# Performance work log

Measured on AMD Instinct MI355X. Metric: run time of the kernel, lower is better.

## Reference

```python
import jax, jax.numpy as jnp
import numpy as np

X_DIM, Z_DIM, N_HEIGHT = 256, 256, 32
EPS = 1e-5  # BatchNorm1d eps

def _bn(x, g, b):
    # BatchNorm1d in training mode: batch statistics over the point axis
    m = x.mean(0)
    v = x.var(0)
    return (x - m) * jax.lax.rsqrt(v + EPS) * g + b

def setup_inputs() -> dict:
    key = jax.random.key(0)
    ks = jax.random.split(key, 16)
    B, N, F = 2, 120000, 3
    inp = {
        'pt_fea': jax.random.normal(ks[0], (B, N, F), jnp.float32),
        'grid_ind': jax.random.randint(ks[1], (B, N, 2), 0, 256, dtype=jnp.int32).astype(jnp.int64),
        'occupancy': (jax.random.uniform(ks[2], (B, 1, X_DIM, N_HEIGHT, Z_DIM)) < 0.1).astype(jnp.float32),
    }
    dims = [(3, 64), (64, 128), (128, 256), (256, 512)]
    for i, (di, do) in enumerate(dims):
        inp[f'W{i+1}'] = jax.random.normal(ks[3 + i], (di, do), jnp.float32) * 0.02
        inp[f'b{i+1}'] = jnp.zeros((do,), jnp.float32)
    for i, d in enumerate([3, 64, 128, 256]):
        inp[f'g{i}'] = jnp.ones((d,), jnp.float32)
        inp[f'be{i}'] = jnp.zeros((d,), jnp.float32)
    inp['Wc'] = jax.random.normal(ks[10], (512, 32), jnp.float32) * 0.02
    inp['bc'] = jnp.zeros((32,), jnp.float32)
    return inp

def reference(pt_fea, occupancy, W1, b1, W2, b2, W3, b3, W4, b4,
              g0, be0, g1, be1, g2, be2, g3, be3, Wc, bc, grid_ind):
    B, N, F = pt_fea.shape
    feats = pt_fea.reshape(B * N, F)                          # cat over batch
    # PointNet per-point MLP: BN -> (Linear -> BN -> ReLU) x3 -> Linear
    h = _bn(feats, g0, be0)
    h = jax.nn.relu(_bn(h @ W1 + b1, g1, be1))
    h = jax.nn.relu(_bn(h @ W2 + b2, g2, be2))
    h = jax.nn.relu(_bn(h @ W3 + b3, g3, be3))
    h = h @ W4 + b4                                           # [B*N, 512]

    # linear segment id per (batch, x, z) cell; equivalent to unique+scatter_max
    gi = grid_ind.reshape(B * N, 2).astype(jnp.int32)
    batch_idx = jnp.repeat(jnp.arange(B, dtype=jnp.int32), N)
    seg = batch_idx * (X_DIM * Z_DIM) + gi[:, 0] * Z_DIM + gi[:, 1]
    n_cells = B * X_DIM * Z_DIM

    pooled = jax.ops.segment_max(h, seg, num_segments=n_cells)          # [cells, 512]
    cnt = jax.ops.segment_sum(jnp.ones((B * N,), h.dtype), seg, num_segments=n_cells)
    occ_mask = (cnt > 0)[:, None]
    pooled = jnp.where(occ_mask, pooled, 0.0)                           # kill -inf empties

    # feature compression on occupied cells only; empty cells stay exactly 0
    comp = jax.nn.relu(pooled @ Wc + bc)
    comp = jnp.where(occ_mask, comp, 0.0)                               # [cells, 32]

    bev = comp.reshape(B, X_DIM, Z_DIM, -1).transpose(0, 3, 1, 2)       # [B, 32, X, Z]
    # MaxPool2d(k=3, stride=1, pad=1); -inf padding matches torch's implicit -inf pad
    bev = jax.lax.reduce_window(bev, -jnp.inf, jax.lax.max,
                                (1, 1, 3, 3), (1, 1, 1, 1), 'SAME')

    occu = occupancy[:, 0].transpose(0, 2, 1, 3)                        # [B, H, X, Z]
    out = jnp.concatenate([occu, bev], axis=1)                          # [B, H+32, X, Z]
    return out
```

## Files before the change

### kernel.cpp

```cpp
#include <hip/hip_runtime.h>
#include <hip/hip_bf16.h>

#define EPSN 1e-5f

typedef __bf16 bf16x8 __attribute__((ext_vector_type(8)));
typedef float f32x4 __attribute__((ext_vector_type(4)));

__device__ __forceinline__ unsigned encf(float f) {
  unsigned u = __float_as_uint(f);
  return (u & 0x80000000u) ? ~u : (u | 0x80000000u);
}
__device__ __forceinline__ float decf(unsigned u) {
  return (u & 0x80000000u) ? __uint_as_float(u ^ 0x80000000u) : __uint_as_float(~u);
}

__global__ __launch_bounds__(256) void stats_feats(const float* __restrict__ pt, int n,
                                                   float* __restrict__ sums) {
  float a0 = 0, a1 = 0, a2 = 0, q0 = 0, q1 = 0, q2 = 0;
  for (int p = blockIdx.x * 256 + threadIdx.x; p < n; p += gridDim.x * 256) {
    float v0 = pt[3 * p], v1 = pt[3 * p + 1], v2 = pt[3 * p + 2];
    a0 += v0; a1 += v1; a2 += v2;
    q0 += v0 * v0; q1 += v1 * v1; q2 += v2 * v2;
  }
  __shared__ float red[4][6];
  float vals[6] = {a0, a1, a2, q0, q1, q2};
  int lane = threadIdx.x & 63, wv = threadIdx.x >> 6;
#pragma unroll
  for (int k = 0; k < 6; k++) {
    float v = vals[k];
#pragma unroll
    for (int o = 32; o; o >>= 1) v += __shfl_down(v, o, 64);
    if (lane == 0) red[wv][k] = v;
  }
  __syncthreads();
  if (threadIdx.x < 6) {
    float v = red[0][threadIdx.x] + red[1][threadIdx.x] + red[2][threadIdx.x] + red[3][threadIdx.x];
    atomicAdd(&sums[threadIdx.x], v);
  }
}

__global__ void bn_prep(const float* __restrict__ sums, int C, float invN,
                        const float* __restrict__ g, const float* __restrict__ be,
                        float* __restrict__ sc, float* __restrict__ sh) {
  int c = threadIdx.x;
  if (c < C) {
    float m = sums[c] * invN;
    float v = fmaxf(sums[C + c] * invN - m * m, 0.f);
    float s = g[c] * rsqrtf(v + EPSN);
    sc[c] = s;
    sh[c] = be[c] - m * s;
  }
}

__global__ __launch_bounds__(256) void wconv(const float* __restrict__ W,
                                             __hip_bfloat16* __restrict__ Wt, int K, int C) {
  int idx = blockIdx.x * 256 + threadIdx.x;
  if (idx >= K * C) return;
  int k = idx / C, c = idx - k * C;
  Wt[(size_t)c * K + k] = __float2bfloat16(W[idx]);
}

__global__ __launch_bounds__(256) void gemm1_stats(const float* __restrict__ pt,
                                                   const float* __restrict__ W,
                                                   const float* __restrict__ bias,
                                                   const float* __restrict__ scsh,
                                                   __hip_bfloat16* __restrict__ Y,
                                                   int n, float* __restrict__ sums) {
  const int c = threadIdx.x & 63;
  const float w0 = W[c], w1 = W[64 + c], w2 = W[128 + c], bb = bias[c];
  const float s0 = scsh[0], s1 = scsh[1], s2 = scsh[2];
  const float h0 = scsh[4], h1 = scsh[5], h2 = scsh[6];
  float s = 0.f, q = 0.f;
  const int total = n * 64;
  for (int idx = blockIdx.x * 256 + threadIdx.x; idx < total; idx += gridDim.x * 256) {
    int p = idx >> 6;
    float x0 = s0 * pt[3 * p]     + h0;
    float x1 = s1 * pt[3 * p + 1] + h1;
    float x2 = s2 * pt[3 * p + 2] + h2;
    float y = bb + x0 * w0 + x1 * w1 + x2 * w2;
    Y[idx] = __float2bfloat16(y);
    s += y; q += y * y;
  }
  __shared__ float sred[4][64], qred[4][64];
  int wv = threadIdx.x >> 6;
  sred[wv][c] = s; qred[wv][c] = q;
  __syncthreads();
  if (threadIdx.x < 64) {
    float S = sred[0][c] + sred[1][c] + sred[2][c] + sred[3][c];
    float Q = qred[0][c] + qred[1][c] + qred[2][c] + qred[3][c];
    atomicAdd(&sums[c], S);
    atomicAdd(&sums[64 + c], Q);
  }
}

template <int K>
__global__ __launch_bounds__(256) void gemm_mfma(
    const __hip_bfloat16* __restrict__ Yin, const __hip_bfloat16* __restrict__ Wt,
    const float* __restrict__ bias, const float* __restrict__ sc, const float* __restrict__ sh,
    __hip_bfloat16* __restrict__ Yout, int C, float* __restrict__ sums, int nrows,
    const unsigned* __restrict__ perm) {
  constexpr int KS = 64, LDA = 72, LDO = 80;
  __shared__ __align__(16) __hip_bfloat16 hA[128 * LDO];
  __shared__ float sredArr[128], qredArr[128];
  const int t = threadIdx.x;
  const int lane = t & 63, wv = t >> 6;
  const int mh = (wv >> 1) * 64, nh = (wv & 1) * 64;
  const int lm = lane & 15, lq = lane >> 4;
  const int p0 = blockIdx.x * 128;
  const int cb0 = blockIdx.y * 128;

  f32x4 acc[4][4];
#pragma unroll
  for (int i = 0; i < 4; i++)
#pragma unroll
    for (int j = 0; j < 4; j++) acc[i][j] = {0.f, 0.f, 0.f, 0.f};

  for (int k0 = 0; k0 < K; k0 += KS) {
    __syncthreads();
#pragma unroll
    for (int it = 0; it < 4; it++) {
      int idx = it * 256 + t;
      int row = idx >> 3;
      int c8 = (idx & 7) * 8;
      int gp = p0 + row;
      __hip_bfloat16 h8[8];
      if (gp < nrows) {
        uint4 raw = *(const uint4*)(Yin + (size_t)gp * K + k0 + c8);
        const __hip_bfloat16* pr = (const __hip_bfloat16*)&raw;
#pragma unroll
        for (int j = 0; j < 8; j++) {
          float v = sc[k0 + c8 + j] * __bfloat162float(pr[j]) + sh[k0 + c8 + j];
          h8[j] = __float2bfloat16(fmaxf(v, 0.f));
        }
      } else {
#pragma unroll
        for (int j = 0; j < 8; j++) h8[j] = __float2bfloat16(0.f);
      }
      *(uint4*)&hA[row * LDA + c8] = *(const uint4*)h8;
    }
    __syncthreads();
#pragma unroll
    for (int kk = 0; kk < KS; kk += 32) {
      bf16x8 a[4], b[4];
#pragma unroll
      for (int i = 0; i < 4; i++)
        a[i] = *(const bf16x8*)&hA[(mh + i * 16 + lm) * LDA + kk + lq * 8];
#pragma unroll
      for (int j = 0; j < 4; j++)
        b[j] = *(const bf16x8*)(const void*)(Wt + (size_t)(cb0 + nh + j * 16 + lm) * K + k0 + kk + lq * 8);
#pragma unroll
      for (int i = 0; i < 4; i++)
#pragma unroll
        for (int j = 0; j < 4; j++)
          acc[i][j] = __builtin_amdgcn_mfma_f32_16x16x32_bf16(a[i], b[j], acc[i][j], 0, 0, 0);
    }
  }

#pragma unroll
  for (int j = 0; j < 4; j++) {
    float bb = bias[cb0 + nh + j * 16 + lm];
#pragma unroll
    for (int i = 0; i < 4; i++)
#pragma unroll
      for (int r = 0; r < 4; r++) acc[i][j][r] += bb;
  }

  __syncthreads();
  if (t < 128) { sredArr[t] = 0.f; qredArr[t] = 0.f; }
  __syncthreads();

#pragma unroll
  for (int j = 0; j < 4; j++) {
    float s = 0.f, q = 0.f;
#pragma unroll
    for (int i = 0; i < 4; i++)
#pragma unroll
      for (int r = 0; r < 4; r++) {
        int grow = p0 + mh + i * 16 + lq * 4 + r;
        if (grow < nrows) { float v = acc[i][j][r]; s += v; q += v * v; }
      }
    s += __shfl_xor(s, 16); s += __shfl_xor(s, 32);
    q += __shfl_xor(q, 16); q += __shfl_xor(q, 32);
    if (lq == 0) {
      atomicAdd(&sredArr[nh + j * 16 + lm], s);
      atomicAdd(&qredArr[nh + j * 16 + lm], q);
    }
  }

  for (int half = 0; half < 2; half++) {
    __syncthreads();
    if ((wv & 1) == half) {
#pragma unroll
      for (int j = 0; j < 4; j++)
#pragma unroll
        for (int i = 0; i < 4; i++)
#pragma unroll
          for (int r = 0; r < 4; r++)
            hA[(mh + i * 16 + lq * 4 + r) * LDO + j * 16 + lm] = __float2bfloat16(acc[i][j][r]);
    }
    __syncthreads();
    int row = t >> 1, seg = t & 1;
    int gp = p0 + row;
    if (gp < nrows) {
      size_t drow = perm ? (size_t)perm[gp] : (size_t)gp;
      const uint4* src = (const uint4*)&hA[row * LDO + seg * 32];
      uint4* dst = (uint4*)(Yout + drow * C + cb0 + half * 64 + seg * 32);
      dst[0] = src[0]; dst[1] = src[1]; dst[2] = src[2]; dst[3] = src[3];
    }
  }

  if (t < 128) {
    atomicAdd(&sums[cb0 + t], sredArr[t]);
    atomicAdd(&sums[C + cb0 + t], qredArr[t]);
  }
}

__global__ __launch_bounds__(256) void hist_kernel(const int* __restrict__ gi, int perB,
                                                   unsigned* __restrict__ hist) {
  int b = blockIdx.y;
  int p = blockIdx.x * 256 + threadIdx.x;
  if (p < perB) {
    int gp = b * perB + p;
    int c = (gi[2 * gp] & 255) * 256 + (gi[2 * gp + 1] & 255);
    atomicAdd(&hist[b * 65536 + c], 1u);
  }
}
__global__ __launch_bounds__(256) void scan1(const unsigned* __restrict__ hist,
                                             unsigned* __restrict__ cursor,
                                             unsigned* __restrict__ bSums) {
  __shared__ unsigned s[256];
  int b = blockIdx.y;
  int t = threadIdx.x, i = b * 65536 + blockIdx.x * 256 + t;
  unsigned v = hist[i]; s[t] = v; __syncthreads();
  for (int off = 1; off < 256; off <<= 1) {
    unsigned x = (t >= off) ? s[t - off] : 0u; __syncthreads();
    s[t] += x; __syncthreads();
  }
  cursor[i] = s[t] - v;
  if (t == 255) bSums[b * 256 + blockIdx.x] = s[255];
}
__global__ void scan2(unsigned* __restrict__ bSums) {
  __shared__ unsigned s[256];
  int t = threadIdx.x, i = blockIdx.x * 256 + t;
  unsigned v = bSums[i]; s[t] = v; __syncthreads();
  for (int off = 1; off < 256; off <<= 1) {
    unsigned x = (t >= off) ? s[t - off] : 0u; __syncthreads();
    s[t] += x; __syncthreads();
  }
  bSums[i] = s[t] - v;
}
__global__ __launch_bounds__(256) void mk_starts(const unsigned* __restrict__ cursor,
                                                 const unsigned* __restrict__ bSums,
                                                 unsigned* __restrict__ starts, int perB) {
  int b = blockIdx.y;
  int i = blockIdx.x * 256 + threadIdx.x;
  starts[b * 65537 + i] = cursor[b * 65536 + i] + bSums[b * 256 + (i >> 8)];
  if (i == 0) starts[b * 65537 + 65536] = (unsigned)perB;
}
__global__ __launch_bounds__(256) void scatter_kernel(const int* __restrict__ gi, int perB,
                                                      unsigned* __restrict__ cursor,
                                                      const unsigned* __restrict__ bSums,
                                                      unsigned* __restrict__ cells,
                                                      unsigned* __restrict__ invPos) {
  int b = blockIdx.y;
  int p = blockIdx.x * 256 + threadIdx.x;
  if (p < perB) {
    int gp = b * perB + p;
    int c = (gi[2 * gp] & 255) * 256 + (gi[2 * gp + 1] & 255);
    unsigned pos = atomicAdd(&cursor[b * 65536 + c], 1u) + bSums[b * 256 + (c >> 8)];
    if (pos >= (unsigned)perB) pos = (unsigned)perB - 1u;
    cells[b * perB + pos] = (unsigned)c;
    invPos[gp] = (unsigned)(b * perB) + pos;
  }
}

__global__ __launch_bounds__(256, 2) void pool_compress(
    const __hip_bfloat16* __restrict__ Y3, const __hip_bfloat16* __restrict__ Wt4,
    const float* __restrict__ b4, const float* __restrict__ sc, const float* __restrict__ sh,
    const __hip_bfloat16* __restrict__ WcT, const float* __restrict__ bc,
    const unsigned* __restrict__ sortedCell, const unsigned* __restrict__ startsAll,
    float* __restrict__ comp, int perB) {
  constexpr int K = 256, KS = 64, LDA = 72, MLW = 516;
  __shared__ __align__(16) __hip_bfloat16 hA[64 * LDA];
  __shared__ __align__(16) unsigned maxLds[32 * MLW];
  __shared__ unsigned char slotRow[256];
  const int t = threadIdx.x;
  const int lane = t & 63, wv = t >> 6;
  const int lm = lane & 15, lq = lane >> 4;
  const int batch = blockIdx.y;
  const unsigned* starts = startsAll + batch * 65537;
  const int c0 = blockIdx.x * 32;
  const int r0 = (int)starts[c0];
  int n = (int)starts[c0 + 32] - r0;
  if (n > 256) n = 256;
  if (n < 0) n = 0;
  const int nrg = (n + 63) >> 6;
  const size_t rowBase = (size_t)batch * perB + r0;

  for (int i = t; i < n; i += 256)
    slotRow[i] = (unsigned char)((sortedCell[batch * perB + r0 + i] - c0) & 31);
  for (int i = t; i < 32 * MLW; i += 256) maxLds[i] = 0u;

  for (int rg = 0; rg < nrg; rg++) {
    const int rbase = rg * 64;
    f32x4 acc[4][8];
#pragma unroll
    for (int i = 0; i < 4; i++)
#pragma unroll
      for (int j = 0; j < 8; j++) acc[i][j] = {0.f, 0.f, 0.f, 0.f};
    for (int k0 = 0; k0 < K; k0 += KS) {
      __syncthreads();
#pragma unroll
      for (int it = 0; it < 2; it++) {
        int idx = it * 256 + t;
        int row = idx >> 3;
        int c8 = (idx & 7) * 8;
        int gr = rbase + row;
        __hip_bfloat16 h8[8];
        if (gr < n) {
          uint4 raw = *(const uint4*)(Y3 + (rowBase + gr) * K + k0 + c8);
          const __hip_bfloat16* pr = (const __hip_bfloat16*)&raw;
#pragma unroll
          for (int j = 0; j < 8; j++) {
            float v = sc[k0 + c8 + j] * __bfloat162float(pr[j]) + sh[k0 + c8 + j];
            h8[j] = __float2bfloat16(fmaxf(v, 0.f));
          }
        } else {
#pragma unroll
          for (int j = 0; j < 8; j++) h8[j] = __float2bfloat16(0.f);
        }
        *(uint4*)&hA[row * LDA + c8] = *(const uint4*)h8;
      }
      __syncthreads();
#pragma unroll
      for (int kk = 0; kk < KS; kk += 32) {
        bf16x8 a[4];
#pragma unroll
        for (int i = 0; i < 4; i++)
          a[i] = *(const bf16x8*)&hA[(i * 16 + lm) * LDA + kk + lq * 8];
#pragma unroll
        for (int j = 0; j < 8; j++) {
          bf16x8 b = *(const bf16x8*)(const void*)(Wt4 + (size_t)(wv * 128 + j * 16 + lm) * K + k0 + kk + lq * 8);
#pragma unroll
          for (int i = 0; i < 4; i++)
            acc[i][j] = __builtin_amdgcn_mfma_f32_16x16x32_bf16(a[i], b, acc[i][j], 0, 0, 0);
        }
      }
    }
#pragma unroll
    for (int j = 0; j < 8; j++) {
      int col = wv * 128 + j * 16 + lm;
#pragma unroll
      for (int i = 0; i < 4; i++) {
#pragma unroll
        for (int r = 0; r < 4; r++) {
          int lrow = rbase + i * 16 + lq * 4 + r;
          if (lrow < n)
            atomicMax(&maxLds[(int)slotRow[lrow] * MLW + col], encf(acc[i][j][r]));
        }
      }
    }
  }
  __syncthreads();

  if (wv < 2) {
    f32x4 accC[2];
    accC[0] = {0.f, 0.f, 0.f, 0.f};
    accC[1] = {0.f, 0.f, 0.f, 0.f};
#pragma unroll
    for (int ks = 0; ks < 16; ks++) {
      int koff = ks * 32 + lq * 8;
      const unsigned* mp = &maxLds[(wv * 16 + lm) * MLW + koff];
      uint4 m0 = *(const uint4*)mp;
      uint4 m1 = *(const uint4*)(mp + 4);
      unsigned mu[8] = {m0.x, m0.y, m0.z, m0.w, m1.x, m1.y, m1.z, m1.w};
      __hip_bfloat16 af[8];
#pragma unroll
      for (int j = 0; j < 8; j++)
        af[j] = __float2bfloat16(decf(mu[j]) + b4[koff + j]);
      bf16x8 aa = *(const bf16x8*)af;
#pragma unroll
      for (int jn = 0; jn < 2; jn++) {
        bf16x8 b = *(const bf16x8*)(const void*)(WcT + (size_t)(jn * 16 + lm) * 512 + koff);
        accC[jn] = __builtin_amdgcn_mfma_f32_16x16x32_bf16(aa, b, accC[jn], 0, 0, 0);
      }
    }
#pragma unroll
    for (int jn = 0; jn < 2; jn++) {
      float bb = bc[jn * 16 + lm];
#pragma unroll
      for (int r = 0; r < 4; r++) {
        int cell = c0 + wv * 16 + lq * 4 + r;
        int occ = starts[cell + 1] > starts[cell];
        float v = occ ? fmaxf(accC[jn][r] + bb, 0.f) : 0.f;
        comp[((size_t)batch * 65536 + cell) * 32 + jn * 16 + lm] = v;
      }
    }
  }
}

__global__ __launch_bounds__(256) void maxpool_write(const float* __restrict__ comp,
                                                     float* __restrict__ out) {
  __shared__ float tile[32][65];
  int bid = blockIdx.x;
  int z0 = (bid & 3) * 64, x = (bid >> 2) & 255, b = bid >> 10;
  int f = threadIdx.x & 31, zs = threadIdx.x >> 5;
  for (int zi = 0; zi < 8; zi++) {
    int z = z0 + zi * 8 + zs;
    float m = -3.402823466e38f;
    for (int dx = -1; dx <= 1; dx++) {
      int xx = x + dx;
      if (xx < 0 || xx > 255) continue;
      for (int dz = -1; dz <= 1; dz++) {
        int zz = z + dz;
        if (zz < 0 || zz > 255) continue;
        m = fmaxf(m, comp[(size_t)((b << 16) + (xx << 8) + zz) * 32 + f]);
      }
    }
    tile[f][zi * 8 + zs] = m;
  }
  __syncthreads();
  int f2 = threadIdx.x >> 3, seg = threadIdx.x & 7;
  float* dst = out + ((size_t)(b * 64 + 32 + f2) * 256 + x) * 256 + z0 + seg * 8;
#pragma unroll
  for (int u = 0; u < 8; u++) dst[u] = tile[f2][seg * 8 + u];
}

__global__ __launch_bounds__(256) void occu_write(const float* __restrict__ occ,
                                                  float* __restrict__ out) {
  int idx = blockIdx.x * 256 + threadIdx.x;
  int z = idx & 255, x = (idx >> 8) & 255, hh = (idx >> 16) & 31, b = idx >> 21;
  out[((size_t)(b * 64 + hh) * 256 + x) * 256 + z] =
      occ[((size_t)((b * 256 + x) * 32 + hh)) * 256 + z];
}

extern "C" void kernel_launch(void* const* d_in, const int* in_sizes, int n_in,
                              void* d_out, int out_size, void* d_ws, size_t ws_size,
                              hipStream_t stream) {
  const float* pt_fea   = (const float*)d_in[0];
  const int*   grid_ind = (const int*)d_in[1];
  const float* occup    = (const float*)d_in[2];
  const float* W1 = (const float*)d_in[3];  const float* b1 = (const float*)d_in[4];
  const float* W2 = (const float*)d_in[5];  const float* b2 = (const float*)d_in[6];
  const float* W3 = (const float*)d_in[7];  const float* b3 = (const float*)d_in[8];
  const float* W4 = (const float*)d_in[9];  const float* b4 = (const float*)d_in[10];
  const float* g0 = (const float*)d_in[11]; const float* be0 = (const float*)d_in[12];
  const float* g1 = (const float*)d_in[13]; const float* be1 = (const float*)d_in[14];
  const float* g2 = (const float*)d_in[15]; const float* be2 = (const float*)d_in[16];
  const float* g3 = (const float*)d_in[17]; const float* be3 = (const float*)d_in[18];
  const float* Wc = (const float*)d_in[19]; const float* bc = (const float*)d_in[20];
  float* out = (float*)d_out;

  const int nPts = in_sizes[0] / 3;
  const int perB = nPts / 2;
  const float invN = 1.f / (float)nPts;

  char* ws = (char*)d_ws;
  float* stats = (float*)ws;
  float* scsh  = (float*)(ws + 4096);
  float* sums0 = stats;        float* sums1 = stats + 16;
  float* sums2 = stats + 160;  float* sums3 = stats + 416;
  float* sc0 = scsh;
  float* sc1 = scsh + 16;   float* sh1 = scsh + 80;
  float* sc2 = scsh + 144;  float* sh2 = scsh + 272;
  float* sc3 = scsh + 400;  float* sh3 = scsh + 656;
  __hip_bfloat16* Wt2 = (__hip_bfloat16*)(ws + 8192);
  __hip_bfloat16* Wt3 = (__hip_bfloat16*)(ws + 24576);
  __hip_bfloat16* Wt4 = (__hip_bfloat16*)(ws + 90112);
  __hip_bfloat16* WcT = (__hip_bfloat16*)(ws + 352256);
  char* S0 = ws + 385024;
  __hip_bfloat16* Y1 = (__hip_bfloat16*)S0;
  __hip_bfloat16* Y2 = (__hip_bfloat16*)(S0 + 30720000ll);
  __hip_bfloat16* Y3 = (__hip_bfloat16*)(S0 + 92160000ll);
  float* comp       = (float*)S0;
  char* sortBase    = S0 + 17000000ll;
  unsigned* hist    = (unsigned*)sortBase;
  unsigned* cursor  = hist + 2 * 65536;
  unsigned* bSums   = cursor + 2 * 65536;
  unsigned* startsA = bSums + 1024;
  unsigned* cells   = startsA + 131080;
  unsigned* invPos  = cells + 2 * perB;

  hipMemsetAsync(stats, 0, 4096, stream);

  wconv<<<(64 * 128 + 255) / 256, 256, 0, stream>>>(W2, Wt2, 64, 128);
  wconv<<<(128 * 256 + 255) / 256, 256, 0, stream>>>(W3, Wt3, 128, 256);
  wconv<<<(256 * 512 + 255) / 256, 256, 0, stream>>>(W4, Wt4, 256, 512);
  wconv<<<(512 * 32 + 255) / 256, 256, 0, stream>>>(Wc, WcT, 512, 32);

  stats_feats<<<256, 256, 0, stream>>>(pt_fea, nPts, sums0);
  bn_prep<<<1, 256, 0, stream>>>(sums0, 3, invN, g0, be0, sc0, scsh + 4);

  gemm1_stats<<<512, 256, 0, stream>>>(pt_fea, W1, b1, scsh, Y1, nPts, sums1);
  bn_prep<<<1, 256, 0, stream>>>(sums1, 64, invN, g1, be1, sc1, sh1);

  gemm_mfma<64><<<dim3(nPts / 128, 1), 256, 0, stream>>>(Y1, Wt2, b2, sc1, sh1, Y2, 128, sums2, nPts, nullptr);
  bn_prep<<<1, 256, 0, stream>>>(sums2, 128, invN, g2, be2, sc2, sh2);

  hipMemsetAsync(hist, 0, 2 * 65536 * 4, stream);
  const int pgrid = (perB + 255) / 256;
  hist_kernel<<<dim3(pgrid, 2), 256, 0, stream>>>(grid_ind, perB, hist);
  scan1<<<dim3(256, 2), 256, 0, stream>>>(hist, cursor, bSums);
  scan2<<<2, 256, 0, stream>>>(bSums);
  mk_starts<<<dim3(256, 2), 256, 0, stream>>>(cursor, bSums, startsA, perB);
  scatter_kernel<<<dim3(pgrid, 2), 256, 0, stream>>>(grid_ind, perB, cursor, bSums, cells, invPos);

  gemm_mfma<128><<<dim3(nPts / 128, 2), 256, 0, stream>>>(Y2, Wt3, b3, sc2, sh2, Y3, 256, sums3, nPts, invPos);
  bn_prep<<<1, 256, 0, stream>>>(sums3, 256, invN, g3, be3, sc3, sh3);

  pool_compress<<<dim3(2048, 2), 256, 0, stream>>>(
      Y3, Wt4, b4, sc3, sh3, WcT, bc, cells, startsA, comp, perB);

  maxpool_write<<<2048, 256, 0, stream>>>(comp, out);
  occu_write<<<16384, 256, 0, stream>>>(occup, out);
}
```

Measured before the change: 723.9 us.

## Apply BN3+ReLU in separate pass and load A fragments directly from global

```diff
diff --git a/kernel.cpp b/kernel.cpp
--- a/kernel.cpp
+++ b/kernel.cpp
@@ -215,6 +215,23 @@
   }
 }
 
+__global__ __launch_bounds__(256) void bn3_apply(__hip_bfloat16* __restrict__ Y,
+                                                 const float* __restrict__ sc,
+                                                 const float* __restrict__ sh, long total8) {
+  for (long i = blockIdx.x * 256 + threadIdx.x; i < total8; i += (long)gridDim.x * 256) {
+    uint4 raw = *(const uint4*)(Y + i * 8);
+    const __hip_bfloat16* pr = (const __hip_bfloat16*)&raw;
+    const int col = (int)(i & 31) * 8;
+    __hip_bfloat16 h8[8];
+#pragma unroll
+    for (int e = 0; e < 8; e++) {
+      float v = fmaf(sc[col + e], __bfloat162float(pr[e]), sh[col + e]);
+      h8[e] = __float2bfloat16(fmaxf(v, 0.f));
+    }
+    *(uint4*)(Y + i * 8) = *(const uint4*)h8;
+  }
+}
+
 __global__ __launch_bounds__(256) void hist_kernel(const int* __restrict__ gi, int perB,
                                                    unsigned* __restrict__ hist) {
   int b = blockIdx.y;
@@ -276,12 +293,11 @@
 
 __global__ __launch_bounds__(256, 2) void pool_compress(
     const __hip_bfloat16* __restrict__ Y3, const __hip_bfloat16* __restrict__ Wt4,
-    const float* __restrict__ b4, const float* __restrict__ sc, const float* __restrict__ sh,
+    const float* __restrict__ b4,
     const __hip_bfloat16* __restrict__ WcT, const float* __restrict__ bc,
     const unsigned* __restrict__ sortedCell, const unsigned* __restrict__ startsAll,
     float* __restrict__ comp, int perB) {
-  constexpr int K = 256, KS = 64, LDA = 72, MLW = 516;
-  __shared__ __align__(16) __hip_bfloat16 hA[64 * LDA];
+  constexpr int K = 256, MLW = 516;
   __shared__ __align__(16) unsigned maxLds[32 * MLW];
   __shared__ unsigned char slotRow[256];
   const int t = threadIdx.x;
@@ -300,6 +316,7 @@
   for (int i = t; i < n; i += 256)
     slotRow[i] = (unsigned char)((sortedCell[batch * perB + r0 + i] - c0) & 31);
   for (int i = t; i < 32 * MLW; i += 256) maxLds[i] = 0u;
+  __syncthreads();
 
   for (int rg = 0; rg < nrg; rg++) {
     const int rbase = rg * 64;
@@ -308,43 +325,22 @@
     for (int i = 0; i < 4; i++)
 #pragma unroll
       for (int j = 0; j < 8; j++) acc[i][j] = {0.f, 0.f, 0.f, 0.f};
-    for (int k0 = 0; k0 < K; k0 += KS) {
-      __syncthreads();
-#pragma unroll
-      for (int it = 0; it < 2; it++) {
-        int idx = it * 256 + t;
-        int row = idx >> 3;
-        int c8 = (idx & 7) * 8;
-        int gr = rbase + row;
-        __hip_bfloat16 h8[8];
-        if (gr < n) {
-          uint4 raw = *(const uint4*)(Y3 + (rowBase + gr) * K + k0 + c8);
-          const __hip_bfloat16* pr = (const __hip_bfloat16*)&raw;
-#pragma unroll
-          for (int j = 0; j < 8; j++) {
-            float v = sc[k0 + c8 + j] * __bfloat162float(pr[j]) + sh[k0 + c8 + j];
-            h8[j] = __float2bfloat16(fmaxf(v, 0.f));
-          }
-        } else {
-#pragma unroll
-          for (int j = 0; j < 8; j++) h8[j] = __float2bfloat16(0.f);
-        }
-        *(uint4*)&hA[row * LDA + c8] = *(const uint4*)h8;
-      }
-      __syncthreads();
-#pragma unroll
-      for (int kk = 0; kk < KS; kk += 32) {
-        bf16x8 a[4];
+
+#pragma unroll 2
+    for (int kk = 0; kk < K; kk += 32) {
+      bf16x8 a[4];
+#pragma unroll
+      for (int i = 0; i < 4; i++) {
+        int gr = rbase + i * 16 + lm;
+        int grc = gr < n ? gr : n - 1;
+        a[i] = *(const bf16x8*)(const void*)(Y3 + (rowBase + grc) * K + kk + lq * 8);
+      }
+#pragma unroll
+      for (int j = 0; j < 8; j++) {
+        bf16x8 b = *(const bf16x8*)(const void*)(Wt4 + (size_t)(wv * 128 + j * 16 + lm) * K + kk + lq * 8);
 #pragma unroll
         for (int i = 0; i < 4; i++)
-          a[i] = *(const bf16x8*)&hA[(i * 16 + lm) * LDA + kk + lq * 8];
-#pragma unroll
-        for (int j = 0; j < 8; j++) {
-          bf16x8 b = *(const bf16x8*)(const void*)(Wt4 + (size_t)(wv * 128 + j * 16 + lm) * K + k0 + kk + lq * 8);
-#pragma unroll
-          for (int i = 0; i < 4; i++)
-            acc[i][j] = __builtin_amdgcn_mfma_f32_16x16x32_bf16(a[i], b, acc[i][j], 0, 0, 0);
-        }
+          acc[i][j] = __builtin_amdgcn_mfma_f32_16x16x32_bf16(a[i], b, acc[i][j], 0, 0, 0);
       }
     }
 #pragma unroll
@@ -508,8 +504,10 @@
   gemm_mfma<128><<<dim3(nPts / 128, 2), 256, 0, stream>>>(Y2, Wt3, b3, sc2, sh2, Y3, 256, sums3, nPts, invPos);
   bn_prep<<<1, 256, 0, stream>>>(sums3, 256, invN, g3, be3, sc3, sh3);
 
+  bn3_apply<<<2048, 256, 0, stream>>>(Y3, sc3, sh3, (long)nPts * 32);
+
   pool_compress<<<dim3(2048, 2), 256, 0, stream>>>(
-      Y3, Wt4, b4, sc3, sh3, WcT, bc, cells, startsA, comp, perB);
+      Y3, Wt4, b4, WcT, bc, cells, startsA, comp, perB);
 
   maxpool_write<<<2048, 256, 0, stream>>>(comp, out);
   occu_write<<<16384, 256, 0, stream>>>(occup, out);
```

Measured after the change: 784.9 us. 1.08x slower.

## Replace LDS atomicMax pooling with per-cell segmented max over bf16 tile

Applied to the files above, without the earlier changes.

```diff
diff --git a/kernel.cpp b/kernel.cpp
--- a/kernel.cpp
+++ b/kernel.cpp
@@ -5,14 +5,6 @@
 
 typedef __bf16 bf16x8 __attribute__((ext_vector_type(8)));
 typedef float f32x4 __attribute__((ext_vector_type(4)));
-
-__device__ __forceinline__ unsigned encf(float f) {
-  unsigned u = __float_as_uint(f);
-  return (u & 0x80000000u) ? ~u : (u | 0x80000000u);
-}
-__device__ __forceinline__ float decf(unsigned u) {
-  return (u & 0x80000000u) ? __uint_as_float(u ^ 0x80000000u) : __uint_as_float(~u);
-}
 
 __global__ __launch_bounds__(256) void stats_feats(const float* __restrict__ pt, int n,
                                                    float* __restrict__ sums) {
@@ -260,7 +252,6 @@
 __global__ __launch_bounds__(256) void scatter_kernel(const int* __restrict__ gi, int perB,
                                                       unsigned* __restrict__ cursor,
                                                       const unsigned* __restrict__ bSums,
-                                                      unsigned* __restrict__ cells,
                                                       unsigned* __restrict__ invPos) {
   int b = blockIdx.y;
   int p = blockIdx.x * 256 + threadIdx.x;
@@ -269,7 +260,6 @@
     int c = (gi[2 * gp] & 255) * 256 + (gi[2 * gp + 1] & 255);
     unsigned pos = atomicAdd(&cursor[b * 65536 + c], 1u) + bSums[b * 256 + (c >> 8)];
     if (pos >= (unsigned)perB) pos = (unsigned)perB - 1u;
-    cells[b * perB + pos] = (unsigned)c;
     invPos[gp] = (unsigned)(b * perB) + pos;
   }
 }
@@ -278,41 +268,46 @@
     const __hip_bfloat16* __restrict__ Y3, const __hip_bfloat16* __restrict__ Wt4,
     const float* __restrict__ b4, const float* __restrict__ sc, const float* __restrict__ sh,
     const __hip_bfloat16* __restrict__ WcT, const float* __restrict__ bc,
-    const unsigned* __restrict__ sortedCell, const unsigned* __restrict__ startsAll,
-    float* __restrict__ comp, int perB) {
-  constexpr int K = 256, KS = 64, LDA = 72, MLW = 516;
-  __shared__ __align__(16) __hip_bfloat16 hA[64 * LDA];
-  __shared__ __align__(16) unsigned maxLds[32 * MLW];
-  __shared__ unsigned char slotRow[256];
+    const unsigned* __restrict__ startsAll, float* __restrict__ comp, int perB) {
+  constexpr int K = 256, KS = 64, LDA = 72, TLW = 520, MR = 48, MAXN = 192;
+  __shared__ __align__(16) __hip_bfloat16 tile[MR * TLW];
+  __hip_bfloat16* hA = tile;
+  __shared__ int cellRow[17];
   const int t = threadIdx.x;
   const int lane = t & 63, wv = t >> 6;
   const int lm = lane & 15, lq = lane >> 4;
   const int batch = blockIdx.y;
   const unsigned* starts = startsAll + batch * 65537;
-  const int c0 = blockIdx.x * 32;
+  const int c0 = blockIdx.x * 16;
   const int r0 = (int)starts[c0];
-  int n = (int)starts[c0 + 32] - r0;
-  if (n > 256) n = 256;
+  int n = (int)starts[c0 + 16] - r0;
+  if (n > MAXN) n = MAXN;
   if (n < 0) n = 0;
-  const int nrg = (n + 63) >> 6;
+  const int nrg = (n + MR - 1) / MR;
   const size_t rowBase = (size_t)batch * perB + r0;
 
-  for (int i = t; i < n; i += 256)
-    slotRow[i] = (unsigned char)((sortedCell[batch * perB + r0 + i] - c0) & 31);
-  for (int i = t; i < 32 * MLW; i += 256) maxLds[i] = 0u;
+  if (t < 17) {
+    int v = (int)starts[c0 + t] - r0;
+    cellRow[t] = v < n ? v : n;
+  }
+
+  const int cid = t >> 4;
+  const int cb0r = (t & 15) * 32;
+  float mx[32];
+#pragma unroll
+  for (int k = 0; k < 32; k++) mx[k] = -3.402823466e38f;
 
   for (int rg = 0; rg < nrg; rg++) {
-    const int rbase = rg * 64;
-    f32x4 acc[4][8];
-#pragma unroll
-    for (int i = 0; i < 4; i++)
+    const int rbase = rg * MR;
+    f32x4 acc[3][8];
+#pragma unroll
+    for (int i = 0; i < 3; i++)
 #pragma unroll
       for (int j = 0; j < 8; j++) acc[i][j] = {0.f, 0.f, 0.f, 0.f};
+
     for (int k0 = 0; k0 < K; k0 += KS) {
       __syncthreads();
-#pragma unroll
-      for (int it = 0; it < 2; it++) {
-        int idx = it * 256 + t;
+      for (int idx = t; idx < MR * 8; idx += 256) {
         int row = idx >> 3;
         int c8 = (idx & 7) * 8;
         int gr = rbase + row;
@@ -321,80 +316,96 @@
           uint4 raw = *(const uint4*)(Y3 + (rowBase + gr) * K + k0 + c8);
           const __hip_bfloat16* pr = (const __hip_bfloat16*)&raw;
 #pragma unroll
-          for (int j = 0; j < 8; j++) {
-            float v = sc[k0 + c8 + j] * __bfloat162float(pr[j]) + sh[k0 + c8 + j];
-            h8[j] = __float2bfloat16(fmaxf(v, 0.f));
+          for (int e = 0; e < 8; e++) {
+            float v = fmaf(sc[k0 + c8 + e], __bfloat162float(pr[e]), sh[k0 + c8 + e]);
+            h8[e] = __float2bfloat16(fmaxf(v, 0.f));
           }
         } else {
 #pragma unroll
-          for (int j = 0; j < 8; j++) h8[j] = __float2bfloat16(0.f);
+          for (int e = 0; e < 8; e++) h8[e] = __float2bfloat16(0.f);
         }
         *(uint4*)&hA[row * LDA + c8] = *(const uint4*)h8;
       }
       __syncthreads();
 #pragma unroll
       for (int kk = 0; kk < KS; kk += 32) {
-        bf16x8 a[4];
-#pragma unroll
-        for (int i = 0; i < 4; i++)
+        bf16x8 a[3];
+#pragma unroll
+        for (int i = 0; i < 3; i++)
           a[i] = *(const bf16x8*)&hA[(i * 16 + lm) * LDA + kk + lq * 8];
 #pragma unroll
         for (int j = 0; j < 8; j++) {
           bf16x8 b = *(const bf16x8*)(const void*)(Wt4 + (size_t)(wv * 128 + j * 16 + lm) * K + k0 + kk + lq * 8);
 #pragma unroll
-          for (int i = 0; i < 4; i++)
+          for (int i = 0; i < 3; i++)
             acc[i][j] = __builtin_amdgcn_mfma_f32_16x16x32_bf16(a[i], b, acc[i][j], 0, 0, 0);
         }
       }
     }
-#pragma unroll
-    for (int j = 0; j < 8; j++) {
-      int col = wv * 128 + j * 16 + lm;
-#pragma unroll
-      for (int i = 0; i < 4; i++) {
-#pragma unroll
-        for (int r = 0; r < 4; r++) {
-          int lrow = rbase + i * 16 + lq * 4 + r;
-          if (lrow < n)
-            atomicMax(&maxLds[(int)slotRow[lrow] * MLW + col], encf(acc[i][j][r]));
+    __syncthreads();
+#pragma unroll
+    for (int i = 0; i < 3; i++)
+#pragma unroll
+      for (int j = 0; j < 8; j++) {
+        int col = wv * 128 + j * 16 + lm;
+#pragma unroll
+        for (int r = 0; r < 4; r++)
+          tile[(i * 16 + lq * 4 + r) * TLW + col] = __float2bfloat16(acc[i][j][r]);
+      }
+    __syncthreads();
+    {
+      int lo = cellRow[cid] - rbase;
+      int hi = cellRow[cid + 1] - rbase;
+      if (lo < 0) lo = 0;
+      if (hi > MR) hi = MR;
+      for (int row = lo; row < hi; row++) {
+        const __hip_bfloat16* p = &tile[row * TLW + cb0r];
+#pragma unroll
+        for (int q = 0; q < 4; q++) {
+          uint4 m = *(const uint4*)(p + q * 8);
+          const __hip_bfloat16* pm = (const __hip_bfloat16*)&m;
+#pragma unroll
+          for (int e = 0; e < 8; e++)
+            mx[q * 8 + e] = fmaxf(mx[q * 8 + e], __bfloat162float(pm[e]));
         }
       }
     }
   }
+
+  __syncthreads();
+  {
+#pragma unroll
+    for (int q = 0; q < 4; q++) {
+      __hip_bfloat16 h8[8];
+#pragma unroll
+      for (int e = 0; e < 8; e++) h8[e] = __float2bfloat16(mx[q * 8 + e]);
+      *(uint4*)&tile[cid * TLW + cb0r + q * 8] = *(const uint4*)h8;
+    }
+  }
   __syncthreads();
 
   if (wv < 2) {
-    f32x4 accC[2];
-    accC[0] = {0.f, 0.f, 0.f, 0.f};
-    accC[1] = {0.f, 0.f, 0.f, 0.f};
+    f32x4 accC = {0.f, 0.f, 0.f, 0.f};
 #pragma unroll
     for (int ks = 0; ks < 16; ks++) {
       int koff = ks * 32 + lq * 8;
-      const unsigned* mp = &maxLds[(wv * 16 + lm) * MLW + koff];
-      uint4 m0 = *(const uint4*)mp;
-      uint4 m1 = *(const uint4*)(mp + 4);
-      unsigned mu[8] = {m0.x, m0.y, m0.z, m0.w, m1.x, m1.y, m1.z, m1.w};
+      uint4 m = *(const uint4*)&tile[lm * TLW + koff];
+      const __hip_bfloat16* pm = (const __hip_bfloat16*)&m;
       __hip_bfloat16 af[8];
 #pragma unroll
       for (int j = 0; j < 8; j++)
-        af[j] = __float2bfloat16(decf(mu[j]) + b4[koff + j]);
+        af[j] = __float2bfloat16(__bfloat162float(pm[j]) + b4[koff + j]);
       bf16x8 aa = *(const bf16x8*)af;
-#pragma unroll
-      for (int jn = 0; jn < 2; jn++) {
-        bf16x8 b = *(const bf16x8*)(const void*)(WcT + (size_t)(jn * 16 + lm) * 512 + koff);
-        accC[jn] = __builtin_amdgcn_mfma_f32_16x16x32_bf16(aa, b, accC[jn], 0, 0, 0);
-      }
-    }
-#pragma unroll
-    for (int jn = 0; jn < 2; jn++) {
-      float bb = bc[jn * 16 + lm];
-#pragma unroll
-      for (int r = 0; r < 4; r++) {
-        int cell = c0 + wv * 16 + lq * 4 + r;
-        int occ = starts[cell + 1] > starts[cell];
-        float v = occ ? fmaxf(accC[jn][r] + bb, 0.f) : 0.f;
-        comp[((size_t)batch * 65536 + cell) * 32 + jn * 16 + lm] = v;
-      }
+      bf16x8 b = *(const bf16x8*)(const void*)(WcT + (size_t)(wv * 16 + lm) * 512 + koff);
+      accC = __builtin_amdgcn_mfma_f32_16x16x32_bf16(aa, b, accC, 0, 0, 0);
+    }
+    float bb = bc[wv * 16 + lm];
+#pragma unroll
+    for (int r = 0; r < 4; r++) {
+      int cell = c0 + lq * 4 + r;
+      int occ = starts[cell + 1] > starts[cell];
+      float v = occ ? fmaxf(accC[r] + bb, 0.f) : 0.f;
+      comp[((size_t)batch * 65536 + cell) * 32 + wv * 16 + lm] = v;
     }
   }
 }
@@ -478,8 +489,7 @@
   unsigned* cursor  = hist + 2 * 65536;
   unsigned* bSums   = cursor + 2 * 65536;
   unsigned* startsA = bSums + 1024;
-  unsigned* cells   = startsA + 131080;
-  unsigned* invPos  = cells + 2 * perB;
+  unsigned* invPos  = startsA + 131080;
 
   hipMemsetAsync(stats, 0, 4096, stream);
 
@@ -503,13 +513,13 @@
   scan1<<<dim3(256, 2), 256, 0, stream>>>(hist, cursor, bSums);
   scan2<<<2, 256, 0, stream>>>(bSums);
   mk_starts<<<dim3(256, 2), 256, 0, stream>>>(cursor, bSums, startsA, perB);
-  scatter_kernel<<<dim3(pgrid, 2), 256, 0, stream>>>(grid_ind, perB, cursor, bSums, cells, invPos);
+  scatter_kernel<<<dim3(pgrid, 2), 256, 0, stream>>>(grid_ind, perB, cursor, bSums, invPos);
 
   gemm_mfma<128><<<dim3(nPts / 128, 2), 256, 0, stream>>>(Y2, Wt3, b3, sc2, sh2, Y3, 256, sums3, nPts, invPos);
   bn_prep<<<1, 256, 0, stream>>>(sums3, 256, invN, g3, be3, sc3, sh3);
 
-  pool_compress<<<dim3(2048, 2), 256, 0, stream>>>(
-      Y3, Wt4, b4, sc3, sh3, WcT, bc, cells, startsA, comp, perB);
+  pool_compress<<<dim3(4096, 2), 256, 0, stream>>>(
+      Y3, Wt4, b4, sc3, sh3, WcT, bc, startsA, comp, perB);
 
   maxpool_write<<<2048, 256, 0, stream>>>(comp, out);
   occu_write<<<16384, 256, 0, stream>>>(occup, out);
```

After: 1.221 ms. 1.69x slower.
